# Kernel optimization log

Measured on AMD Instinct MI355X. Metric: run time of the kernel, lower is better.

## Reference

```python
import jax, jax.numpy as jnp
import numpy as np
import math

B, S, D, H = 2, 2048, 1024, 16
DK = D // H


def setup_inputs() -> dict:
    key = jax.random.key(0)
    ks = jax.random.split(key, 12)
    scale = 1.0 / math.sqrt(D)
    inp = {
        'query': jax.random.normal(ks[0], (B, S, D), dtype=jnp.float32),
        'key': jax.random.normal(ks[1], (B, S, D), dtype=jnp.float32),
        'value': jax.random.normal(ks[2], (B, S, D), dtype=jnp.float32),
        'mask': jnp.ones((B, 1, S), dtype=jnp.int32),
        'posr': jax.random.normal(ks[3], (B, S, S), dtype=jnp.float32),
        'Wq': jax.random.normal(ks[4], (D, D), dtype=jnp.float32) * scale,
        'bq': jnp.zeros((D,), dtype=jnp.float32),
        'Wk': jax.random.normal(ks[5], (D, D), dtype=jnp.float32) * scale,
        'bk': jnp.zeros((D,), dtype=jnp.float32),
        'Wv': jax.random.normal(ks[6], (D, D), dtype=jnp.float32) * scale,
        'bv': jnp.zeros((D,), dtype=jnp.float32),
        'Wo': jax.random.normal(ks[7], (D, D), dtype=jnp.float32) * scale,
        'bo': jnp.zeros((D,), dtype=jnp.float32),
    }
    return inp


def _split_heads(x):
    # [B, S, D] -> [B, H, S, DK]
    b, s, _ = x.shape
    return x.reshape(b, s, H, DK).transpose(0, 2, 1, 3)


def reference(query, key, value, mask, posr, Wq, bq, Wk, bk, Wv, bv, Wo, bo):
    q = _split_heads(query @ Wq.T + bq)   # [B,H,S,DK]
    k = _split_heads(key @ Wk.T + bk)
    v = _split_heads(value @ Wv.T + bv)

    scores = jnp.einsum('bhqd,bhkd->bhqk', q, k) / math.sqrt(DK)
    scores = scores + posr[:, None, :, :]            # additive positional bias
    m = mask[:, None, :, :]                           # [B,1,1,S] broadcast
    scores = jnp.where(m == 0, jnp.float32(-1e9), scores)
    p = jax.nn.softmax(scores, axis=-1)
    ctx = jnp.einsum('bhqk,bhkd->bhqd', p, v)        # [B,H,S,DK]
    ctx = ctx.transpose(0, 2, 1, 3).reshape(query.shape[0], -1, D)
    return ctx @ Wo.T + bo
```

## Files before the change

### kernel.cpp

```cpp
#include <hip/hip_runtime.h>
#include <math.h>

#define B_ 2
#define S_ 2048
#define D_ 1024
#define H_ 16
#define DK_ 64

typedef __attribute__((ext_vector_type(8))) short bf16x8;
typedef __attribute__((ext_vector_type(4))) float f32x4;

#define MFMA16(a, b, c) __builtin_amdgcn_mfma_f32_16x16x32_bf16((a), (b), (c), 0, 0, 0)

#define ASYNC16(g, l)                                                          \
    __builtin_amdgcn_global_load_lds(                                          \
        (const __attribute__((address_space(1))) void*)(g),                    \
        (__attribute__((address_space(3))) void*)(l), 16, 0, 0)

#define LOG2E 1.4426950408889634f

__device__ __forceinline__ unsigned short f2bf(float x) {
    unsigned int u = __float_as_uint(x);
    unsigned int r = (u + 0x7fffu + ((u >> 16) & 1u)) >> 16;
    return (unsigned short)r;
}

__global__ __launch_bounds__(256)
void pack_all(const float* __restrict__ q, const float* __restrict__ k,
              const float* __restrict__ v, const float* __restrict__ wq,
              const float* __restrict__ wk, const float* __restrict__ wv,
              const float* __restrict__ wo, unsigned short* __restrict__ ws0)
{
    const int z = blockIdx.z;
    const size_t IN = 4194304, WT = 1048576;
    const float* in;
    unsigned short* dst;
    int n;
    switch (z) {
        case 0: in = q;  dst = ws0;            n = (int)IN; break;
        case 1: in = k;  dst = ws0 + IN;       n = (int)IN; break;
        case 2: in = v;  dst = ws0 + 2*IN;     n = (int)IN; break;
        case 3: in = wq; dst = ws0 + 3*IN;          n = (int)WT; break;
        case 4: in = wk; dst = ws0 + 3*IN + WT;     n = (int)WT; break;
        case 5: in = wv; dst = ws0 + 3*IN + 2*WT;   n = (int)WT; break;
        default:in = wo; dst = ws0 + 3*IN + 3*WT;   n = (int)WT; break;
    }
    const int n4 = n >> 2;
    const int stride = gridDim.x * blockDim.x;
    for (int i = blockIdx.x * blockDim.x + threadIdx.x; i < n4; i += stride) {
        float4 x = ((const float4*)in)[i];
        ushort4 hv;
        hv.x = f2bf(x.x); hv.y = f2bf(x.y); hv.z = f2bf(x.z); hv.w = f2bf(x.w);
        ((ushort4*)dst)[i] = hv;
    }
}

__device__ __forceinline__ void gemm_core2ph(
    const unsigned short* __restrict__ A, const unsigned short* __restrict__ B,
    unsigned short (*As)[128 * 64], unsigned short (*Bs)[64 * 64],
    int m0, int n0, f32x4 (&acc)[4][2])
{
    const int tid  = threadIdx.x;
    const int w    = tid >> 6;
    const int lane = tid & 63;
    const int rA   = lane & 15;
    const int quad = lane >> 4;
    const int wm   = (w & 1) * 64;
    const int wn   = (w >> 1) * 32;

    const int rowc = tid >> 3;
    const int gc   = (tid & 7) ^ (rowc & 7);

#define STA(buf, k0) do {                                                       \
        _Pragma("unroll")                                                       \
        for (int i_ = 0; i_ < 4; ++i_)                                          \
            ASYNC16(A + (size_t)(m0 + i_ * 32 + rowc) * 1024 + (k0) + gc * 8,   \
                    &As[buf][(size_t)(i_ * 256 + w * 64) * 8]);                 \
    } while (0)
#define STB(buf, k0) do {                                                       \
        _Pragma("unroll")                                                       \
        for (int i_ = 0; i_ < 2; ++i_)                                          \
            ASYNC16(B + (size_t)(n0 + i_ * 32 + rowc) * 1024 + (k0) + gc * 8,   \
                    &Bs[buf][(size_t)(i_ * 256 + w * 64) * 8]);                 \
    } while (0)

    STA(0, 0);
    STB(0, 0);
    __syncthreads();

#pragma unroll 1
    for (int k = 0; k < 16; ++k) {
        const int cur = k & 1;
        if (k < 15) {
            STA(cur ^ 1, (k + 1) * 64);
            STB(cur ^ 1, (k + 1) * 64);
        }
#pragma unroll
        for (int ks = 0; ks < 2; ++ks) {
            bf16x8 a[4], bb[2];
#pragma unroll
            for (int mt = 0; mt < 4; ++mt) {
                const int row = wm + mt * 16 + rA;
                a[mt] = *(const bf16x8*)
                    &As[cur][row * 64 + (((ks * 4 + quad) ^ (row & 7)) * 8)];
            }
#pragma unroll
            for (int nt = 0; nt < 2; ++nt) {
                const int row = wn + nt * 16 + rA;
                bb[nt] = *(const bf16x8*)
                    &Bs[cur][row * 64 + (((ks * 4 + quad) ^ (row & 7)) * 8)];
            }
#pragma unroll
            for (int mt = 0; mt < 4; ++mt)
#pragma unroll
                for (int nt = 0; nt < 2; ++nt)
                    acc[mt][nt] = MFMA16(a[mt], bb[nt], acc[mt][nt]);
        }
        __syncthreads();
    }
#undef STA
#undef STB
}

__device__ __forceinline__ void swz512(int& m0, int& n0) {
    const int bid = (int)(blockIdx.x + (blockIdx.y << 4));
    const int swz = (bid & 7) * 64 + (bid >> 3);
    m0 = (swz >> 4) * 128;
    n0 = (swz & 15) * 64;
}

__global__ __launch_bounds__(256, 3)
void gemm_qkv(const unsigned short* __restrict__ ws0,
              const float* __restrict__ bq, const float* __restrict__ bk,
              const float* __restrict__ bv,
              unsigned short* __restrict__ qbuf, unsigned short* __restrict__ kbuf,
              unsigned short* __restrict__ vtbuf)
{
    __shared__ unsigned short As[2][128 * 64];
    __shared__ unsigned short Bs[2][64 * 64];
    const size_t IN = 4194304, WT = 1048576;
    const int z = blockIdx.z;
    const unsigned short* Ap = ws0 + (size_t)z * IN;
    const unsigned short* Bp = ws0 + 3 * IN + (size_t)z * WT;
    const float* bias = (z == 0) ? bq : (z == 1) ? bk : bv;
    unsigned short* dst = (z == 0) ? qbuf : (z == 1) ? kbuf : vtbuf;

    int m0, n0;
    swz512(m0, n0);
    f32x4 acc[4][2] = {};
    gemm_core2ph(Ap, Bp, As, Bs, m0, n0, acc);

    const int tid = threadIdx.x, w = tid >> 6, lane = tid & 63;
    const int quad = lane >> 4, col = lane & 15;
    const int wm = (w & 1) * 64, wn = (w >> 1) * 32;

    if (z == 2) {
        unsigned short* Ts = &As[0][0];
#pragma unroll
        for (int mt = 0; mt < 4; ++mt)
#pragma unroll
            for (int nt = 0; nt < 2; ++nt) {
                const int ln  = wn + nt * 16 + col;
                const int lmb = wm + mt * 16 + quad * 4;
                const float bv_ = bias[n0 + ln];
                ushort4 h;
                h.x = f2bf(acc[mt][nt][0] + bv_);
                h.y = f2bf(acc[mt][nt][1] + bv_);
                h.z = f2bf(acc[mt][nt][2] + bv_);
                h.w = f2bf(acc[mt][nt][3] + bv_);
                *(ushort4*)&Ts[ln * 128 + (lmb ^ ((ln & 7) << 3))] = h;
            }
        __syncthreads();
        const int d    = tid >> 2;
        const int cg   = (tid & 3) * 32;
        const int bb   = m0 >> 11;
        const int sb   = m0 & 2047;
        const int hh   = n0 >> 6;
        unsigned short* drow =
            dst + ((size_t)(bb * 16 + hh) * 64 + d) * 2048 + sb;
#pragma unroll
        for (int j = 0; j < 8; ++j) {
            const int c = cg + j * 4;
            ushort4 hv = *(const ushort4*)&Ts[d * 128 + (c ^ ((d & 7) << 3))];
            *(ushort4*)&drow[c] = hv;
        }
        return;
    }

    const float qscale = (z == 0) ? (0.125f * LOG2E) : 1.0f;
#pragma unroll
    for (int mt = 0; mt < 4; ++mt)
#pragma unroll
        for (int nt = 0; nt < 2; ++nt) {
            f32x4 v = acc[mt][nt];
#pragma unroll
            for (int r = 0; r < 4; ++r) {
                const int m = m0 + wm + mt * 16 + quad * 4 + r;
                const int n = n0 + wn + nt * 16 + col;
                const float val = (v[r] + bias[n]) * qscale;
                const int bb = m >> 11, ss = m & 2047;
                const int hh = n >> 6, dd = n & 63;
                dst[((size_t)(bb * 16 + hh) * 2048 + ss) * 64 + dd] = f2bf(val);
            }
        }
}

__global__ __launch_bounds__(256, 3)
void gemm_out(const unsigned short* __restrict__ Actx,
              const unsigned short* __restrict__ Bwo,
              const float* __restrict__ bias, float* __restrict__ out)
{
    __shared__ unsigned short As[2][128 * 64];
    __shared__ unsigned short Bs[2][64 * 64];
    int m0, n0;
    swz512(m0, n0);
    f32x4 acc[4][2] = {};
    gemm_core2ph(Actx, Bwo, As, Bs, m0, n0, acc);

    const int tid = threadIdx.x, w = tid >> 6, lane = tid & 63;
    const int quad = lane >> 4, col = lane & 15;
    const int wm = (w & 1) * 64, wn = (w >> 1) * 32;
#pragma unroll
    for (int mt = 0; mt < 4; ++mt)
#pragma unroll
        for (int nt = 0; nt < 2; ++nt) {
            f32x4 v = acc[mt][nt];
#pragma unroll
            for (int r = 0; r < 4; ++r) {
                const int m = m0 + wm + mt * 16 + quad * 4 + r;
                const int n = n0 + wn + nt * 16 + col;
                out[(size_t)m * 1024 + n] = v[r] + bias[n];
            }
        }
}

__global__ __launch_bounds__(256, 2)
void attn_mfma(const unsigned short* __restrict__ qbuf,
               const unsigned short* __restrict__ kbuf,
               const unsigned short* __restrict__ vtbuf,
               const float* __restrict__ posr, const int* __restrict__ mask,
               unsigned short* __restrict__ ctxb)
{
    __shared__ unsigned short Ks[3][64 * 64];
    __shared__ unsigned short Vts[3][64 * 64];
    __shared__ unsigned short Ps[128 * 64];

    const int tid  = threadIdx.x;
    const int w    = tid >> 6;
    const int lane = tid & 63;
    const int quad = lane >> 4;
    const int col  = lane & 15;
    const int q0   = blockIdx.x * 128;
    const int h    = blockIdx.y;
    const int b    = blockIdx.z;
    const int wq   = w * 32;

    const size_t headoff = (size_t)(b * 16 + h) * 2048 * 64;
    const unsigned short* Qh  = qbuf + headoff + (size_t)q0 * 64;
    const unsigned short* Kh  = kbuf + headoff;
    const unsigned short* Vth = vtbuf + headoff;

    const int c0 = tid;
    const int c1 = 256 + tid;
    const int r0 = c0 >> 3, g0 = (c0 & 7) ^ (r0 & 7);
    const int r1 = c1 >> 3, g1 = (c1 & 7) ^ (r1 & 7);

#define STAGE(bufidx, kt) do {                                                  \
        ASYNC16(Kh + (size_t)((kt) * 64 + r0) * 64 + g0 * 8,                    \
                &Ks[bufidx][(size_t)(w * 64) * 8]);                             \
        ASYNC16(Kh + (size_t)((kt) * 64 + r1) * 64 + g1 * 8,                    \
                &Ks[bufidx][(size_t)(256 + w * 64) * 8]);                       \
        ASYNC16(Vth + (size_t)r0 * 2048 + (kt) * 64 + g0 * 8,                   \
                &Vts[bufidx][(size_t)(w * 64) * 8]);                            \
        ASYNC16(Vth + (size_t)r1 * 2048 + (kt) * 64 + g1 * 8,                   \
                &Vts[bufidx][(size_t)(256 + w * 64) * 8]);                      \
    } while (0)

    bf16x8 qf[2][2];
#pragma unroll
    for (int mt = 0; mt < 2; ++mt)
#pragma unroll
        for (int ks = 0; ks < 2; ++ks)
            qf[mt][ks] = *(const bf16x8*)
                &Qh[(size_t)(wq + mt * 16 + col) * 64 + ks * 32 + quad * 8];

    const float* prq[2][4];
#pragma unroll
    for (int mt = 0; mt < 2; ++mt)
#pragma unroll
        for (int r = 0; r < 4; ++r)
            prq[mt][r] = posr +
                ((size_t)b * 2048 + (q0 + wq + mt * 16 + quad * 4 + r)) * 2048;
    const int* mrow = mask + (size_t)b * 2048;

    STAGE(0, 0);
    STAGE(1, 1);

    float pr[2][4][4];
    int   mk[4];
#pragma unroll
    for (int mt = 0; mt < 2; ++mt)
#pragma unroll
        for (int r = 0; r < 4; ++r)
#pragma unroll
            for (int nt = 0; nt < 4; ++nt)
                pr[mt][r][nt] = prq[mt][r][nt * 16 + col];
#pragma unroll
    for (int nt = 0; nt < 4; ++nt) mk[nt] = mrow[nt * 16 + col];

    f32x4 sc[2][4];
    f32x4 O[2][4] = {};
    float lsum[2][4] = {{0.f, 0.f, 0.f, 0.f}, {0.f, 0.f, 0.f, 0.f}};

    __syncthreads();

#pragma unroll
    for (int mt = 0; mt < 2; ++mt)
#pragma unroll
        for (int nt = 0; nt < 4; ++nt) sc[mt][nt] = (f32x4){0.f, 0.f, 0.f, 0.f};
#pragma unroll
    for (int nt = 0; nt < 4; ++nt)
#pragma unroll
        for (int ks = 0; ks < 2; ++ks) {
            const bf16x8 bk = *(const bf16x8*)
                &Ks[0][(nt * 16 + col) * 64 + (((ks * 4 + quad) ^ (col & 7)) * 8)];
#pragma unroll
            for (int mt = 0; mt < 2; ++mt)
                sc[mt][nt] = MFMA16(qf[mt][ks], bk, sc[mt][nt]);
        }

    int bb = 0, b1 = 1, b2 = 2;
#pragma unroll 1
    for (int t = 0; t < 32; ++t) {
#pragma unroll
        for (int mt = 0; mt < 2; ++mt)
#pragma unroll
            for (int r = 0; r < 4; ++r) {
                const int rowW = wq + mt * 16 + quad * 4 + r;
                const int rsw  = rowW & 7;
#pragma unroll
                for (int nt = 0; nt < 4; ++nt) {
                    const float e = __builtin_amdgcn_exp2f(
                        fmaf(pr[mt][r][nt], LOG2E, sc[mt][nt][r]));
                    unsigned int u = __float_as_uint(e) & 0xffff0000u;
                    u = mk[nt] ? u : 0u;
                    lsum[mt][r] += __uint_as_float(u);
                    const int kk = nt * 16 + col;
                    Ps[rowW * 64 + (((kk >> 3) ^ rsw) * 8) + (kk & 7)] =
                        (unsigned short)(u >> 16);
                }
            }

        __builtin_amdgcn_sched_barrier(0);
        asm volatile("s_waitcnt lgkmcnt(0)" ::: "memory");
        __builtin_amdgcn_s_barrier();
        __builtin_amdgcn_sched_barrier(0);

        if (t < 30) STAGE(b2, t + 2);
        __builtin_amdgcn_sched_barrier(0);

        if (t < 31) {
            const int kn = (t + 1) * 64;
#pragma unroll
            for (int mt = 0; mt < 2; ++mt)
#pragma unroll
                for (int r = 0; r < 4; ++r)
#pragma unroll
                    for (int nt = 0; nt < 4; ++nt)
                        pr[mt][r][nt] = prq[mt][r][kn + nt * 16 + col];
#pragma unroll
            for (int nt = 0; nt < 4; ++nt) mk[nt] = mrow[kn + nt * 16 + col];
        }

#pragma unroll
        for (int ks = 0; ks < 2; ++ks) {
            bf16x8 pa[2];
#pragma unroll
            for (int mt = 0; mt < 2; ++mt)
                pa[mt] = *(const bf16x8*)
                    &Ps[(wq + mt * 16 + col) * 64 + (((ks * 4 + quad) ^ (col & 7)) * 8)];
#pragma unroll
            for (int nt = 0; nt < 4; ++nt) {
                const bf16x8 vb = *(const bf16x8*)
                    &Vts[bb][(nt * 16 + col) * 64 + (((ks * 4 + quad) ^ (col & 7)) * 8)];
#pragma unroll
                for (int mt = 0; mt < 2; ++mt)
                    O[mt][nt] = MFMA16(pa[mt], vb, O[mt][nt]);
            }
        }

        if (t < 31) {
#pragma unroll
            for (int mt = 0; mt < 2; ++mt)
#pragma unroll
                for (int nt = 0; nt < 4; ++nt)
                    sc[mt][nt] = (f32x4){0.f, 0.f, 0.f, 0.f};
#pragma unroll
            for (int nt = 0; nt < 4; ++nt)
#pragma unroll
                for (int ks = 0; ks < 2; ++ks) {
                    const bf16x8 bk = *(const bf16x8*)
                        &Ks[b1][(nt * 16 + col) * 64 + (((ks * 4 + quad) ^ (col & 7)) * 8)];
#pragma unroll
                    for (int mt = 0; mt < 2; ++mt)
                        sc[mt][nt] = MFMA16(qf[mt][ks], bk, sc[mt][nt]);
                }
        }
        const int tmp = bb; bb = b1; b1 = b2; b2 = tmp;
    }

#pragma unroll
    for (int mt = 0; mt < 2; ++mt)
#pragma unroll
        for (int r = 0; r < 4; ++r) {
#pragma unroll
            for (int o = 1; o < 16; o <<= 1)
                lsum[mt][r] += __shfl_xor(lsum[mt][r], o);
        }

#pragma unroll
    for (int mt = 0; mt < 2; ++mt)
#pragma unroll
        for (int r = 0; r < 4; ++r) {
            const float inv = 1.f / lsum[mt][r];
            const int rowW = wq + mt * 16 + quad * 4 + r;
            const size_t rowoff =
                ((size_t)b * 2048 + (q0 + rowW)) * 1024 + h * 64;
#pragma unroll
            for (int nt = 0; nt < 4; ++nt)
                ctxb[rowoff + nt * 16 + col] = f2bf(O[mt][nt][r] * inv);
        }
#undef STAGE
}

extern "C" void kernel_launch(void* const* d_in, const int* in_sizes, int n_in,
                              void* d_out, int out_size, void* d_ws, size_t ws_size,
                              hipStream_t stream) {
    const float* query = (const float*)d_in[0];
    const float* key   = (const float*)d_in[1];
    const float* value = (const float*)d_in[2];
    const int*   mask  = (const int*)  d_in[3];
    const float* posr  = (const float*)d_in[4];
    const float* Wq    = (const float*)d_in[5];
    const float* bq    = (const float*)d_in[6];
    const float* Wk    = (const float*)d_in[7];
    const float* bk    = (const float*)d_in[8];
    const float* Wv    = (const float*)d_in[9];
    const float* bv    = (const float*)d_in[10];
    const float* Wo    = (const float*)d_in[11];
    const float* bo    = (const float*)d_in[12];
    float* out = (float*)d_out;

    unsigned short* ws0   = (unsigned short*)d_ws;
    const size_t IN = 4194304, WT = 1048576;
    unsigned short* qbuf  = ws0 + 4 * IN;
    unsigned short* kbuf  = ws0 + 5 * IN;
    unsigned short* vtbuf = ws0 + 6 * IN;
    unsigned short* ctxb  = ws0 + 7 * IN;
    const unsigned short* wob = ws0 + 3 * IN + 3 * WT;

    pack_all<<<dim3(512, 1, 7), 256, 0, stream>>>(query, key, value, Wq, Wk, Wv, Wo, ws0);

    gemm_qkv<<<dim3(16, 32, 3), 256, 0, stream>>>(ws0, bq, bk, bv, qbuf, kbuf, vtbuf);

    attn_mfma<<<dim3(16, 16, 2), 256, 0, stream>>>(qbuf, kbuf, vtbuf, posr, mask, ctxb);

    gemm_out<<<dim3(16, 32), 256, 0, stream>>>(ctxb, wob, bo, out);
}
```

Measured before the change: 259.2 us.

## Enlarge GEMM tiles to 128x128 and compute softmax row sums via MFMA

The QKV and output projection GEMMs move from 128x64 to 128x128 block tiles, with each wave now covering 64x64. This halves the grid, raises operand reuse per load and changes the block swizzle, at the cost of more registers and LDS and lower occupancy (launch bounds go from 3 to 2). In attention, the per-row softmax denominator is now accumulated by an extra MFMA of the bf16 P tile against a vector of ones. This replaces the scalar adds and the cross-lane shuffle reduction, and because the sum is taken over the same bf16-rounded P values used for P·V, normalization stays consistent.

```diff
diff --git a/kernel.cpp b/kernel.cpp
--- a/kernel.cpp
+++ b/kernel.cpp
@@ -57,8 +57,8 @@
 
 __device__ __forceinline__ void gemm_core2ph(
     const unsigned short* __restrict__ A, const unsigned short* __restrict__ B,
-    unsigned short (*As)[128 * 64], unsigned short (*Bs)[64 * 64],
-    int m0, int n0, f32x4 (&acc)[4][2])
+    unsigned short (*As)[128 * 64], unsigned short (*Bs)[128 * 64],
+    int m0, int n0, f32x4 (&acc)[4][4])
 {
     const int tid  = threadIdx.x;
     const int w    = tid >> 6;
@@ -66,7 +66,7 @@
     const int rA   = lane & 15;
     const int quad = lane >> 4;
     const int wm   = (w & 1) * 64;
-    const int wn   = (w >> 1) * 32;
+    const int wn   = (w >> 1) * 64;
 
     const int rowc = tid >> 3;
     const int gc   = (tid & 7) ^ (rowc & 7);
@@ -79,7 +79,7 @@
     } while (0)
 #define STB(buf, k0) do {                                                       \
         _Pragma("unroll")                                                       \
-        for (int i_ = 0; i_ < 2; ++i_)                                          \
+        for (int i_ = 0; i_ < 4; ++i_)                                          \
             ASYNC16(B + (size_t)(n0 + i_ * 32 + rowc) * 1024 + (k0) + gc * 8,   \
                     &Bs[buf][(size_t)(i_ * 256 + w * 64) * 8]);                 \
     } while (0)
@@ -97,7 +97,7 @@
         }
 #pragma unroll
         for (int ks = 0; ks < 2; ++ks) {
-            bf16x8 a[4], bb[2];
+            bf16x8 a[4], bb[4];
 #pragma unroll
             for (int mt = 0; mt < 4; ++mt) {
                 const int row = wm + mt * 16 + rA;
@@ -105,7 +105,7 @@
                     &As[cur][row * 64 + (((ks * 4 + quad) ^ (row & 7)) * 8)];
             }
 #pragma unroll
-            for (int nt = 0; nt < 2; ++nt) {
+            for (int nt = 0; nt < 4; ++nt) {
                 const int row = wn + nt * 16 + rA;
                 bb[nt] = *(const bf16x8*)
                     &Bs[cur][row * 64 + (((ks * 4 + quad) ^ (row & 7)) * 8)];
@@ -113,7 +113,7 @@
 #pragma unroll
             for (int mt = 0; mt < 4; ++mt)
 #pragma unroll
-                for (int nt = 0; nt < 2; ++nt)
+                for (int nt = 0; nt < 4; ++nt)
                     acc[mt][nt] = MFMA16(a[mt], bb[nt], acc[mt][nt]);
         }
         __syncthreads();
@@ -122,14 +122,14 @@
 #undef STB
 }
 
-__device__ __forceinline__ void swz512(int& m0, int& n0) {
-    const int bid = (int)(blockIdx.x + (blockIdx.y << 4));
-    const int swz = (bid & 7) * 64 + (bid >> 3);
-    m0 = (swz >> 4) * 128;
-    n0 = (swz & 15) * 64;
-}
-
-__global__ __launch_bounds__(256, 3)
+__device__ __forceinline__ void swz256(int& m0, int& n0) {
+    const int bid = (int)(blockIdx.x + (blockIdx.y << 3));
+    const int swz = (bid & 7) * 32 + (bid >> 3);
+    m0 = (swz >> 3) * 128;
+    n0 = (swz & 7) * 128;
+}
+
+__global__ __launch_bounds__(256, 2)
 void gemm_qkv(const unsigned short* __restrict__ ws0,
               const float* __restrict__ bq, const float* __restrict__ bk,
               const float* __restrict__ bv,
@@ -137,7 +137,7 @@
               unsigned short* __restrict__ vtbuf)
 {
     __shared__ unsigned short As[2][128 * 64];
-    __shared__ unsigned short Bs[2][64 * 64];
+    __shared__ unsigned short Bs[2][128 * 64];
     const size_t IN = 4194304, WT = 1048576;
     const int z = blockIdx.z;
     const unsigned short* Ap = ws0 + (size_t)z * IN;
@@ -146,20 +146,20 @@
     unsigned short* dst = (z == 0) ? qbuf : (z == 1) ? kbuf : vtbuf;
 
     int m0, n0;
-    swz512(m0, n0);
-    f32x4 acc[4][2] = {};
+    swz256(m0, n0);
+    f32x4 acc[4][4] = {};
     gemm_core2ph(Ap, Bp, As, Bs, m0, n0, acc);
 
     const int tid = threadIdx.x, w = tid >> 6, lane = tid & 63;
     const int quad = lane >> 4, col = lane & 15;
-    const int wm = (w & 1) * 64, wn = (w >> 1) * 32;
+    const int wm = (w & 1) * 64, wn = (w >> 1) * 64;
 
     if (z == 2) {
         unsigned short* Ts = &As[0][0];
 #pragma unroll
         for (int mt = 0; mt < 4; ++mt)
 #pragma unroll
-            for (int nt = 0; nt < 2; ++nt) {
+            for (int nt = 0; nt < 4; ++nt) {
                 const int ln  = wn + nt * 16 + col;
                 const int lmb = wm + mt * 16 + quad * 4;
                 const float bv_ = bias[n0 + ln];
@@ -171,16 +171,16 @@
                 *(ushort4*)&Ts[ln * 128 + (lmb ^ ((ln & 7) << 3))] = h;
             }
         __syncthreads();
-        const int d    = tid >> 2;
-        const int cg   = (tid & 3) * 32;
+        const int d    = tid >> 1;
+        const int half = (tid & 1) * 64;
         const int bb   = m0 >> 11;
         const int sb   = m0 & 2047;
-        const int hh   = n0 >> 6;
+        const int hh   = (n0 + d) >> 6;
         unsigned short* drow =
-            dst + ((size_t)(bb * 16 + hh) * 64 + d) * 2048 + sb;
-#pragma unroll
-        for (int j = 0; j < 8; ++j) {
-            const int c = cg + j * 4;
+            dst + ((size_t)(bb * 16 + hh) * 64 + (d & 63)) * 2048 + sb;
+#pragma unroll
+        for (int j = 0; j < 16; ++j) {
+            const int c = half + j * 4;
             ushort4 hv = *(const ushort4*)&Ts[d * 128 + (c ^ ((d & 7) << 3))];
             *(ushort4*)&drow[c] = hv;
         }
@@ -191,7 +191,7 @@
 #pragma unroll
     for (int mt = 0; mt < 4; ++mt)
 #pragma unroll
-        for (int nt = 0; nt < 2; ++nt) {
+        for (int nt = 0; nt < 4; ++nt) {
             f32x4 v = acc[mt][nt];
 #pragma unroll
             for (int r = 0; r < 4; ++r) {
@@ -205,25 +205,25 @@
         }
 }
 
-__global__ __launch_bounds__(256, 3)
+__global__ __launch_bounds__(256, 2)
 void gemm_out(const unsigned short* __restrict__ Actx,
               const unsigned short* __restrict__ Bwo,
               const float* __restrict__ bias, float* __restrict__ out)
 {
     __shared__ unsigned short As[2][128 * 64];
-    __shared__ unsigned short Bs[2][64 * 64];
+    __shared__ unsigned short Bs[2][128 * 64];
     int m0, n0;
-    swz512(m0, n0);
-    f32x4 acc[4][2] = {};
+    swz256(m0, n0);
+    f32x4 acc[4][4] = {};
     gemm_core2ph(Actx, Bwo, As, Bs, m0, n0, acc);
 
     const int tid = threadIdx.x, w = tid >> 6, lane = tid & 63;
     const int quad = lane >> 4, col = lane & 15;
-    const int wm = (w & 1) * 64, wn = (w >> 1) * 32;
+    const int wm = (w & 1) * 64, wn = (w >> 1) * 64;
 #pragma unroll
     for (int mt = 0; mt < 4; ++mt)
 #pragma unroll
-        for (int nt = 0; nt < 2; ++nt) {
+        for (int nt = 0; nt < 4; ++nt) {
             f32x4 v = acc[mt][nt];
 #pragma unroll
             for (int r = 0; r < 4; ++r) {
@@ -293,6 +293,9 @@
                 ((size_t)b * 2048 + (q0 + wq + mt * 16 + quad * 4 + r)) * 2048;
     const int* mrow = mask + (size_t)b * 2048;
 
+    const short one = (short)0x3F80;
+    const bf16x8 ones = {one, one, one, one, one, one, one, one};
+
     STAGE(0, 0);
     STAGE(1, 1);
 
@@ -310,7 +313,7 @@
 
     f32x4 sc[2][4];
     f32x4 O[2][4] = {};
-    float lsum[2][4] = {{0.f, 0.f, 0.f, 0.f}, {0.f, 0.f, 0.f, 0.f}};
+    f32x4 lacc[2] = {};
 
     __syncthreads();
 
@@ -342,12 +345,11 @@
                 for (int nt = 0; nt < 4; ++nt) {
                     const float e = __builtin_amdgcn_exp2f(
                         fmaf(pr[mt][r][nt], LOG2E, sc[mt][nt][r]));
-                    unsigned int u = __float_as_uint(e) & 0xffff0000u;
+                    unsigned int u = __float_as_uint(e) >> 16;
                     u = mk[nt] ? u : 0u;
-                    lsum[mt][r] += __uint_as_float(u);
                     const int kk = nt * 16 + col;
                     Ps[rowW * 64 + (((kk >> 3) ^ rsw) * 8) + (kk & 7)] =
-                        (unsigned short)(u >> 16);
+                        (unsigned short)u;
                 }
             }
 
@@ -387,6 +389,9 @@
                 for (int mt = 0; mt < 2; ++mt)
                     O[mt][nt] = MFMA16(pa[mt], vb, O[mt][nt]);
             }
+#pragma unroll
+            for (int mt = 0; mt < 2; ++mt)
+                lacc[mt] = MFMA16(pa[mt], ones, lacc[mt]);
         }
 
         if (t < 31) {
@@ -413,16 +418,7 @@
     for (int mt = 0; mt < 2; ++mt)
 #pragma unroll
         for (int r = 0; r < 4; ++r) {
-#pragma unroll
-            for (int o = 1; o < 16; o <<= 1)
-                lsum[mt][r] += __shfl_xor(lsum[mt][r], o);
-        }
-
-#pragma unroll
-    for (int mt = 0; mt < 2; ++mt)
-#pragma unroll
-        for (int r = 0; r < 4; ++r) {
-            const float inv = 1.f / lsum[mt][r];
+            const float inv = 1.f / lacc[mt][r];
             const int rowW = wq + mt * 16 + quad * 4 + r;
             const size_t rowoff =
                 ((size_t)b * 2048 + (q0 + rowW)) * 1024 + h * 64;
@@ -461,9 +457,9 @@
 
     pack_all<<<dim3(512, 1, 7), 256, 0, stream>>>(query, key, value, Wq, Wk, Wv, Wo, ws0);
 
-    gemm_qkv<<<dim3(16, 32, 3), 256, 0, stream>>>(ws0, bq, bk, bv, qbuf, kbuf, vtbuf);
+    gemm_qkv<<<dim3(8, 32, 3), 256, 0, stream>>>(ws0, bq, bk, bv, qbuf, kbuf, vtbuf);
 
     attn_mfma<<<dim3(16, 16, 2), 256, 0, stream>>>(qbuf, kbuf, vtbuf, posr, mask, ctxb);
 
-    gemm_out<<<dim3(16, 32), 256, 0, stream>>>(ctxb, wob, bo, out);
-}
+    gemm_out<<<dim3(8, 32), 256, 0, stream>>>(ctxb, wob, bo, out);
+}
```

Result: slower. 266.2 us (+2.7%).
